# Performance work log

Measured on AMD Instinct MI355X. Metric: run time of the kernel, lower is better.

Reference implementation:

```python
import jax, jax.numpy as jnp
import numpy as np
import itertools

RCR = 5.2
RCA = 3.5
NUM_SPECIES = 4
EtaR = jnp.asarray(np.array([16.0], np.float32))
ShfR = jnp.asarray(np.linspace(0.9, 5.2, 17, dtype=np.float32)[:-1])   # 16
EtaA = jnp.asarray(np.array([8.0], np.float32))
Zeta = jnp.asarray(np.array([32.0], np.float32))
ShfA = jnp.asarray(np.linspace(0.9, 3.5, 5, dtype=np.float32)[:-1])    # 4
ShfZ = jnp.asarray(((np.arange(8) + 0.5) * np.pi / 8).astype(np.float32))  # 8


def _cutoff_cosine(d, rc):
    return jnp.where(d <= rc, 0.5 * jnp.cos(np.pi * d / rc) + 0.5, 0.0)


def setup_inputs() -> dict:
    key = jax.random.key(0)
    k1, k2 = jax.random.split(key)
    C, A = 8, 96
    species = jax.random.randint(k1, (C, A), 0, NUM_SPECIES)
    # uniform positions in a 12 Angstrom box -> realistic neighbor counts
    coordinates = jax.random.uniform(k2, (C, A, 3), dtype=jnp.float32) * 12.0
    return {"species": species, "coordinates": coordinates}


def reference(species, coordinates):
    C, A, _ = coordinates.shape
    N = A - 1  # every other atom is a candidate neighbor; cutoff fc zeroes far ones
    # neighbor index list excluding self: nidx[i] = (i+1, ..., i+A-1) mod A
    nidx = (np.arange(A)[:, None] + 1 + np.arange(N)[None, :]) % A  # (A, N)

    # vec[c,i,k] = coords[c,i] - coords[c, nidx[i,k]]  (matches torch convention)
    vec = coordinates[:, :, None, :] - coordinates[:, nidx, :]      # (C,A,N,3)
    dist = jnp.linalg.norm(vec, axis=-1)                            # (C,A,N)
    nsp = species[:, nidx]                                          # (C,A,N)

    # ---- radial subAEV terms: eq (3), 0.25 * exp(-eta (d - Rs)^2) * fc ----
    fc_r = _cutoff_cosine(dist, RCR)                                # (C,A,N)
    d_ = dist[..., None, None]                                      # (C,A,N,1,1)
    rterm = 0.25 * jnp.exp(-EtaR[:, None] * (d_ - ShfR[None, :]) ** 2) * fc_r[..., None, None]
    rterm = rterm.reshape(C, A, N, -1)                              # (C,A,N,16)
    mask_r = (nsp[..., None] == jnp.arange(NUM_SPECIES)).astype(rterm.dtype)  # (C,A,N,S)
    radial = jnp.einsum('cans,canf->casf', mask_r, rterm).reshape(C, A, -1)   # (C,A,64)

    # ---- angular subAEV terms: eq (4), over all neighbor pairs ----
    i1, i2 = np.triu_indices(N, 1)                                  # P = N(N-1)/2 pairs
    v1, v2 = vec[:, :, i1], vec[:, :, i2]                           # (C,A,P,3)
    d1, d2 = dist[:, :, i1], dist[:, :, i2]                         # (C,A,P)
    cos_ang = 0.95 * jnp.sum(v1 * v2, -1) / (d1 * d2)
    angles = jnp.arccos(cos_ang)                                    # (C,A,P)
    fcj = _cutoff_cosine(d1, RCA) * _cutoff_cosine(d2, RCA)         # (C,A,P)

    EtaA_b = EtaA.reshape(-1, 1, 1, 1)
    Zeta_b = Zeta.reshape(1, -1, 1, 1)
    ShfA_b = ShfA.reshape(1, 1, -1, 1)
    ShfZ_b = ShfZ.reshape(1, 1, 1, -1)
    ang_ = angles[..., None, None, None, None]
    dm_ = ((d1 + d2) / 2)[..., None, None, None, None]
    factor1 = ((1 + jnp.cos(ang_ - ShfZ_b)) / 2) ** Zeta_b
    factor2 = jnp.exp(-EtaA_b * (dm_ - ShfA_b) ** 2)
    aterm = 2 * factor1 * factor2 * fcj[..., None, None, None, None]
    P = i1.shape[0]
    aterm = aterm.reshape(C, A, P, -1)                              # (C,A,P,32)

    sp1, sp2 = nsp[:, :, i1], nsp[:, :, i2]                         # (C,A,P)
    pairs = list(itertools.combinations_with_replacement(range(NUM_SPECIES), 2))
    mask_a = jnp.stack([((sp1 == s1) & (sp2 == s2)) | ((sp1 == s2) & (sp2 == s1))
                        for s1, s2 in pairs], axis=-1).astype(aterm.dtype)  # (C,A,P,10)
    angular = jnp.einsum('capq,capf->caqf', mask_a, aterm).reshape(C, A, -1)  # (C,A,320)

    return jnp.concatenate([radial, angular], axis=-1)              # (C,A,384)
```

## Files before the change

kernel.cpp:

```cpp
#include <hip/hip_runtime.h>
#include <math.h>

#define NA 96
#define NN 95
#define F_RCR 5.2f
#define F_RCA 3.5f
#define F_PI 3.14159265358979323846f


__global__ __launch_bounds__(128) void aev_kernel(const int* __restrict__ species,
                                                  const float* __restrict__ coords,
                                                  float* __restrict__ out) {
    const int blk = blockIdx.x;
    const int c = blk / NA;
    const int a = blk % NA;
    const int tid = threadIdx.x;

    __shared__ float scoord[NA * 3];
    __shared__ int ssp[NA];
    __shared__ float cfx[NN], cfy[NN], cfz[NN], cfd[NN], cfc[NN];
    __shared__ int cfs[NN];
    __shared__ int Mcnt;
    __shared__ float rad[64];
    __shared__ float ang[320];

    {
        const float4* src = (const float4*)(coords + (size_t)c * NA * 3);
        float4* dst = (float4*)scoord;
        if (tid < 72) dst[tid] = src[tid];
    }
    for (int i = tid; i < NA; i += 128) ssp[i] = species[c * NA + i];
    for (int i = tid; i < 64; i += 128) rad[i] = 0.0f;
    for (int i = tid; i < 320; i += 128) ang[i] = 0.0f;
    if (tid == 0) Mcnt = 0;
    __syncthreads();

    const float axp = scoord[a * 3 + 0], ayp = scoord[a * 3 + 1], azp = scoord[a * 3 + 2];

    for (int n = tid; n < NN; n += 128) {
        int j = a + 1 + n;
        if (j >= NA) j -= NA;
        const float vx = axp - scoord[j * 3 + 0];
        const float vy = ayp - scoord[j * 3 + 1];
        const float vz = azp - scoord[j * 3 + 2];
        const float d = sqrtf(vx * vx + vy * vy + vz * vz);
        const int sp = ssp[j];
        if (d <= F_RCR) {
            const float fc = 0.5f * __cosf(d * (F_PI / F_RCR)) + 0.5f;
            float* radbase = &rad[sp * 16];
#pragma unroll
            for (int k = 0; k < 16; ++k) {
                const float sh = 0.9f + 0.26875f * (float)k;
                const float dd = d - sh;
                const float term = 0.25f * __expf(-16.0f * dd * dd) * fc;
                atomicAdd(&radbase[k], term);
            }
        }
        if (d <= F_RCA) {
            const int idx = atomicAdd(&Mcnt, 1);
            cfx[idx] = vx;
            cfy[idx] = vy;
            cfz[idx] = vz;
            cfd[idx] = d;
            cfc[idx] = 0.5f * __cosf(d * (F_PI / F_RCA)) + 0.5f;
            cfs[idx] = sp;
        }
    }
    __syncthreads();

    const int M = Mcnt;
    const int npairs = (M * (M - 1)) >> 1;

    const float cZ[8] = {0.98078528f, 0.83146961f, 0.55557023f, 0.19509032f,
                         -0.19509032f, -0.55557023f, -0.83146961f, -0.98078528f};
    const float sZ[8] = {0.19509032f, 0.55557023f, 0.83146961f, 0.98078528f,
                         0.98078528f, 0.83146961f, 0.55557023f, 0.19509032f};

    for (int p = tid; p < npairs; p += 128) {
        int i = (int)((float)(2 * M - 1) * 0.5f -
                      0.5f * sqrtf((float)((2 * M - 1) * (2 * M - 1)) - 8.0f * (float)p));
        if (i < 0) i = 0;
        if (i > M - 2) i = M - 2;
        while (i > 0 && p < (i * (2 * M - i - 1)) / 2) --i;
        while (p >= ((i + 1) * (2 * M - i - 2)) / 2) ++i;
        const int j = i + 1 + (p - (i * (2 * M - i - 1)) / 2);

        const float d1 = cfd[i], d2 = cfd[j];
        const float dot = cfx[i] * cfx[j] + cfy[i] * cfy[j] + cfz[i] * cfz[j];
        const float cosang = 0.95f * dot / (d1 * d2);
        const float sinang = sqrtf(1.0f - cosang * cosang);
        const float fcj = cfc[i] * cfc[j];
        const float dm = 0.5f * (d1 + d2);

        float f2[4];
#pragma unroll
        for (int k = 0; k < 4; ++k) {
            const float sh = 0.9f + 0.65f * (float)k;
            const float dd = dm - sh;
            f2[k] = __expf(-8.0f * dd * dd);
        }

        int s1 = cfs[i], s2 = cfs[j];
        if (s1 > s2) { const int t = s1; s1 = s2; s2 = t; }
        const int q = s1 * 4 - (s1 * (s1 - 1)) / 2 + (s2 - s1);
        float* angbase = &ang[q * 32];

#pragma unroll
        for (int t = 0; t < 8; ++t) {
            const float b = 0.5f * (1.0f + cosang * cZ[t] + sinang * sZ[t]);
            const float b2 = b * b;
            const float b4 = b2 * b2;
            const float b8 = b4 * b4;
            const float b16 = b8 * b8;
            const float b32 = b16 * b16;
            const float pre = 2.0f * b32 * fcj;
#pragma unroll
            for (int k = 0; k < 4; ++k) {
                atomicAdd(&angbase[k * 8 + t], pre * f2[k]);
            }
        }
    }
    __syncthreads();

    float4* orow4 = (float4*)(out + (size_t)(c * NA + a) * 384);
    if (tid < 96) {
        float4 v;
        const int base = tid * 4;
        if (base < 64) {
            v.x = rad[base + 0]; v.y = rad[base + 1];
            v.z = rad[base + 2]; v.w = rad[base + 3];
        } else {
            const int b = base - 64;
            v.x = ang[b + 0]; v.y = ang[b + 1];
            v.z = ang[b + 2]; v.w = ang[b + 3];
        }
        orow4[tid] = v;
    }
}

extern "C" void kernel_launch(void* const* d_in, const int* in_sizes, int n_in,
                              void* d_out, int out_size, void* d_ws, size_t ws_size,
                              hipStream_t stream) {
    const int* species = (const int*)d_in[0];
    const float* coords = (const float*)d_in[1];
    float* out = (float*)d_out;
    const int CA = in_sizes[0];
    aev_kernel<<<CA, 128, 0, stream>>>(species, coords, out);
}
```

Measured before the change: 17.05 us.

## Compact radial neighbors and accumulate per-thread radial features without atomics; use 64-thread blocks

Radial neighbors within cutoff are compacted into shared lists, and each of 64 threads then owns one (species, shift) output element, looping over all radial neighbors and accumulating in a register instead of doing shared-memory atomics. Blocks shrink from 128 to 64 threads (one wavefront), which removes the idle second wave but halves the parallelism available to the angular pair loop. The radial loop now touches every neighbor for every thread, with species selection done by predication.

```diff
diff --git a/kernel.cpp b/kernel.cpp
--- a/kernel.cpp
+++ b/kernel.cpp
@@ -8,9 +8,9 @@
 #define F_PI 3.14159265358979323846f
 
 
-__global__ __launch_bounds__(128) void aev_kernel(const int* __restrict__ species,
-                                                  const float* __restrict__ coords,
-                                                  float* __restrict__ out) {
+__global__ __launch_bounds__(64) void aev_kernel(const int* __restrict__ species,
+                                                 const float* __restrict__ coords,
+                                                 float* __restrict__ out) {
     const int blk = blockIdx.x;
     const int c = blk / NA;
     const int a = blk % NA;
@@ -18,26 +18,26 @@
 
     __shared__ float scoord[NA * 3];
     __shared__ int ssp[NA];
+    __shared__ float rfd[NN], rfc[NN];
+    __shared__ int rfs[NN];
     __shared__ float cfx[NN], cfy[NN], cfz[NN], cfd[NN], cfc[NN];
     __shared__ int cfs[NN];
-    __shared__ int Mcnt;
-    __shared__ float rad[64];
+    __shared__ int Mcnt[2];
     __shared__ float ang[320];
 
     {
         const float4* src = (const float4*)(coords + (size_t)c * NA * 3);
         float4* dst = (float4*)scoord;
-        if (tid < 72) dst[tid] = src[tid];
+        for (int i = tid; i < 72; i += 64) dst[i] = src[i];
     }
-    for (int i = tid; i < NA; i += 128) ssp[i] = species[c * NA + i];
-    for (int i = tid; i < 64; i += 128) rad[i] = 0.0f;
-    for (int i = tid; i < 320; i += 128) ang[i] = 0.0f;
-    if (tid == 0) Mcnt = 0;
+    for (int i = tid; i < NA; i += 64) ssp[i] = species[c * NA + i];
+    for (int i = tid; i < 320; i += 64) ang[i] = 0.0f;
+    if (tid < 2) Mcnt[tid] = 0;
     __syncthreads();
 
     const float axp = scoord[a * 3 + 0], ayp = scoord[a * 3 + 1], azp = scoord[a * 3 + 2];
 
-    for (int n = tid; n < NN; n += 128) {
+    for (int n = tid; n < NN; n += 64) {
         int j = a + 1 + n;
         if (j >= NA) j -= NA;
         const float vx = axp - scoord[j * 3 + 0];
@@ -46,18 +46,13 @@
         const float d = sqrtf(vx * vx + vy * vy + vz * vz);
         const int sp = ssp[j];
         if (d <= F_RCR) {
-            const float fc = 0.5f * __cosf(d * (F_PI / F_RCR)) + 0.5f;
-            float* radbase = &rad[sp * 16];
-#pragma unroll
-            for (int k = 0; k < 16; ++k) {
-                const float sh = 0.9f + 0.26875f * (float)k;
-                const float dd = d - sh;
-                const float term = 0.25f * __expf(-16.0f * dd * dd) * fc;
-                atomicAdd(&radbase[k], term);
-            }
+            const int idx = atomicAdd(&Mcnt[1], 1);
+            rfd[idx] = d;
+            rfc[idx] = 0.5f * __cosf(d * (F_PI / F_RCR)) + 0.5f;
+            rfs[idx] = sp;
         }
         if (d <= F_RCA) {
-            const int idx = atomicAdd(&Mcnt, 1);
+            const int idx = atomicAdd(&Mcnt[0], 1);
             cfx[idx] = vx;
             cfy[idx] = vy;
             cfz[idx] = vz;
@@ -68,7 +63,17 @@
     }
     __syncthreads();
 
-    const int M = Mcnt;
+    const int Mr = Mcnt[1];
+    const int mysp = tid >> 4;
+    const float mysh = 0.9f + 0.26875f * (float)(tid & 15);
+    float racc = 0.0f;
+    for (int m = 0; m < Mr; ++m) {
+        const float dd = rfd[m] - mysh;
+        const float val = 0.25f * __expf(-16.0f * dd * dd) * rfc[m];
+        racc += (rfs[m] == mysp) ? val : 0.0f;
+    }
+
+    const int M = Mcnt[0];
     const int npairs = (M * (M - 1)) >> 1;
 
     const float cZ[8] = {0.98078528f, 0.83146961f, 0.55557023f, 0.19509032f,
@@ -76,7 +81,7 @@
     const float sZ[8] = {0.19509032f, 0.55557023f, 0.83146961f, 0.98078528f,
                          0.98078528f, 0.83146961f, 0.55557023f, 0.19509032f};
 
-    for (int p = tid; p < npairs; p += 128) {
+    for (int p = tid; p < npairs; p += 64) {
         int i = (int)((float)(2 * M - 1) * 0.5f -
                       0.5f * sqrtf((float)((2 * M - 1) * (2 * M - 1)) - 8.0f * (float)p));
         if (i < 0) i = 0;
@@ -122,20 +127,11 @@
     }
     __syncthreads();
 
-    float4* orow4 = (float4*)(out + (size_t)(c * NA + a) * 384);
-    if (tid < 96) {
-        float4 v;
-        const int base = tid * 4;
-        if (base < 64) {
-            v.x = rad[base + 0]; v.y = rad[base + 1];
-            v.z = rad[base + 2]; v.w = rad[base + 3];
-        } else {
-            const int b = base - 64;
-            v.x = ang[b + 0]; v.y = ang[b + 1];
-            v.z = ang[b + 2]; v.w = ang[b + 3];
-        }
-        orow4[tid] = v;
-    }
+    float* orow = out + (size_t)(c * NA + a) * 384;
+    orow[tid] = racc;
+    float4* oang4 = (float4*)(orow + 64);
+    const float4* ang4 = (const float4*)ang;
+    for (int i = tid; i < 80; i += 64) oang4[i] = ang4[i];
 }
 
 extern "C" void kernel_launch(void* const* d_in, const int* in_sizes, int n_in,
@@ -145,5 +141,5 @@
     const float* coords = (const float*)d_in[1];
     float* out = (float*)d_out;
     const int CA = in_sizes[0];
-    aev_kernel<<<CA, 128, 0, stream>>>(species, coords, out);
+    aev_kernel<<<CA, 64, 0, stream>>>(species, coords, out);
 }
```

New measurement: 17.00 us. No clear change (-0.3%).
